# Kernel optimization log

Hardware: AMD Instinct MI355X
Metric: run time of the kernel (lower is better)

The kernel has to match this reference:

```python
import jax, jax.numpy as jnp
import numpy as np

N_NODES = 100000


def _sage_conv(x, edge_index, W_l, b_l, W_r):
    # PyG SAGEConv (aggr='mean', root_weight=True, normalize=False):
    # out = lin_l(mean_{j in N(i)} x_j) + lin_r(x_i)
    src, dst = edge_index[0], edge_index[1]
    n = x.shape[0]
    agg = jax.ops.segment_sum(x[src], dst, num_segments=n)
    cnt = jax.ops.segment_sum(jnp.ones((src.shape[0],), x.dtype), dst, num_segments=n)
    agg = agg / jnp.maximum(cnt, 1.0)[:, None]
    return agg @ W_l + b_l + x @ W_r


def setup_inputs() -> dict:
    key = jax.random.key(0)
    ks = jax.random.split(key, 12)
    in_dim, hidden = 384, 128
    x = jax.random.normal(ks[0], (N_NODES, in_dim), dtype=jnp.float32)
    edge_index = jax.random.randint(ks[1], (2, 3200000), 0, N_NODES, dtype=jnp.int32)
    pos_edge_label_index = jax.random.randint(ks[2], (2, 500000), 0, N_NODES, dtype=jnp.int32)
    neg_edge_label_index = jax.random.randint(ks[3], (2, 500000), 0, N_NODES, dtype=jnp.int32)
    s1 = 1.0 / np.sqrt(in_dim)
    s2 = 1.0 / np.sqrt(hidden)
    return {
        "x": x,
        "edge_index": edge_index,
        "pos_edge_label_index": pos_edge_label_index,
        "neg_edge_label_index": neg_edge_label_index,
        "W_l1": jax.random.uniform(ks[4], (in_dim, hidden), jnp.float32, -s1, s1),
        "b_l1": jnp.zeros((hidden,), jnp.float32),
        "W_r1": jax.random.uniform(ks[5], (in_dim, hidden), jnp.float32, -s1, s1),
        "W_l2": jax.random.uniform(ks[6], (hidden, hidden), jnp.float32, -s2, s2),
        "b_l2": jnp.zeros((hidden,), jnp.float32),
        "W_r2": jax.random.uniform(ks[7], (hidden, hidden), jnp.float32, -s2, s2),
        "W_lin": jax.random.uniform(ks[8], (2 * hidden, 1), jnp.float32, -s2, s2),
        "b_lin": jnp.zeros((1,), jnp.float32),
    }


def reference(x, edge_index, pos_edge_label_index, neg_edge_label_index,
              W_l1, b_l1, W_r1, W_l2, b_l2, W_r2, W_lin, b_lin):
    h = _sage_conv(x, edge_index, W_l1, b_l1, W_r1)
    h = jax.nn.relu(h)
    h = _sage_conv(h, edge_index, W_l2, b_l2, W_r2)

    def score(idx):
        pair = jnp.concatenate([h[idx[0]], h[idx[1]]], axis=1)  # [E, 2*hidden]
        return (pair @ W_lin + b_lin).reshape(-1)

    return score(pos_edge_label_index), score(neg_edge_label_index)
```

## Files before the change

kernel.cpp:

```cpp
#include <hip/hip_runtime.h>

#define IN_DIM 384
#define HID    128
#define NPB    256
#define BCAP   16384
#define LCAP   10240

#define AS1 __attribute__((address_space(1)))
#define AS3 __attribute__((address_space(3)))

typedef _Float16 half8 __attribute__((ext_vector_type(8)));
typedef _Float16 half2t __attribute__((ext_vector_type(2)));
typedef __fp16 fp16x2 __attribute__((ext_vector_type(2)));
typedef float floatx4 __attribute__((ext_vector_type(4)));
typedef float floatx2 __attribute__((ext_vector_type(2)));

__global__ void zero_i32(int* __restrict__ p, int n) {
  int i = blockIdx.x * 256 + threadIdx.x;
  if (i < n) p[i] = 0;
}

__global__ __launch_bounds__(512) void partition_kernel(
    const int* __restrict__ src, const int* __restrict__ dst, int E, int nB,
    int* __restrict__ bCur, unsigned* __restrict__ bucketData) {
  __shared__ int hist[391];
  __shared__ int gbase[391];
  const int t = threadIdx.x;
  const int b0 = blockIdx.x * 8192;

  for (int i = t; i < nB; i += 512) hist[i] = 0;
  __syncthreads();
#pragma unroll
  for (int i = 0; i < 16; ++i) {
    int e = b0 + i * 512 + t;
    if (e < E) atomicAdd(&hist[dst[e] >> 8], 1);
  }
  __syncthreads();
  for (int i = t; i < nB; i += 512) {
    int h = hist[i];
    gbase[i] = h ? (i * BCAP + atomicAdd(&bCur[i], h)) : 0;
    hist[i] = 0;
  }
  __syncthreads();
#pragma unroll
  for (int i = 0; i < 16; ++i) {
    int e = b0 + i * 512 + t;
    if (e < E) {
      int d = dst[e];
      int b = d >> 8;
      int r = atomicAdd(&hist[b], 1);
      bucketData[gbase[b] + r] = ((unsigned)(d & 255) << 17) | (unsigned)src[e];
    }
  }
}

__global__ __launch_bounds__(1024) void node_sort3(
    const unsigned* __restrict__ bucketData, const int* __restrict__ bCur,
    int N, int* __restrict__ sorted_src, int* __restrict__ rs, int* __restrict__ re) {
  extern __shared__ unsigned sdata[];
  __shared__ int hist[NPB];
  __shared__ int s[NPB];
  __shared__ int cur[NPB];
  const int b = blockIdx.x;
  const int t = threadIdx.x;
  const int start = b * BCAP;
  const int fill = bCur[b];
  if (t < NPB) hist[t] = 0;
  __syncthreads();
  for (int i = t; i < fill; i += 1024) {
    unsigned d = bucketData[start + i];
    if (i < LCAP) sdata[i] = d;
    atomicAdd(&hist[d >> 17], 1);
  }
  __syncthreads();
  int v = 0;
  if (t < NPB) { v = hist[t]; s[t] = v; }
  __syncthreads();
  for (int off = 1; off < NPB; off <<= 1) {
    int y = (t < NPB && t >= off) ? s[t - off] : 0;
    __syncthreads();
    if (t < NPB) s[t] += y;
    __syncthreads();
  }
  if (t < NPB) {
    int excl = s[t] - v;
    const int node = b * NPB + t;
    if (node < N) {
      rs[node] = start + excl;
      re[node] = start + excl + v;
    }
    cur[t] = start + excl;
  }
  __syncthreads();
  for (int i = t; i < fill; i += 1024) {
    unsigned d = (i < LCAP) ? sdata[i] : bucketData[start + i];
    int p = atomicAdd(&cur[d >> 17], 1);
    sorted_src[p] = (int)(d & 0x1FFFF);
  }
}

__global__ void pack_w2(const float* __restrict__ Wl, const float* __restrict__ Wr,
                        _Float16* __restrict__ Bp) {
  const float* __restrict__ W = blockIdx.z ? Wr : Wl;
  const int tn = blockIdx.x;
  const int ks = blockIdx.y;
  const int KS = gridDim.y;
  const int lane = threadIdx.x;
  const int n = tn * 16 + (lane & 15);
  const int kb = ks * 32 + (lane >> 4) * 8;
  half8 v;
#pragma unroll
  for (int j = 0; j < 8; ++j) v[j] = (_Float16)W[(size_t)(kb + j) * HID + n];
  *(half8*)(Bp + (((size_t)(blockIdx.z * 8 + tn) * KS + ks) * 64 + lane) * 8) = v;
}

__device__ inline half2t cvt_pk(float a, float b) {
  fp16x2 r = __builtin_amdgcn_cvt_pkrtz(a, b);
  union { fp16x2 f; half2t h; } c;
  c.f = r;
  return c.h;
}

__global__ __launch_bounds__(512) void gemm_f32a(
    const float* __restrict__ A, int M,
    const _Float16* __restrict__ Bp,
    unsigned char* __restrict__ y8, _Float16* __restrict__ z1) {
  __shared__ float As[128 * 32];

  const int K = IN_DIM, KS = IN_DIM / 32;
  const int tid = threadIdx.x;
  const int lane = tid & 63;
  const int wid = tid >> 6;
  const int quad = lane >> 4;
  const int lm = lane & 15;
  const int row0 = (wid & 1) * 64;
  const int ct0 = (wid >> 1) * 4;
  const int blockRow = blockIdx.x * 128;

  const int srow = lane >> 3;
  const int scol = ((lane & 7) ^ (srow & 7)) * 4;
  const int grow0 = min(blockRow + wid * 16 + srow, M - 1);
  const int grow1 = min(blockRow + wid * 16 + 8 + srow, M - 1);

  floatx4 acc[16];
#pragma unroll
  for (int i = 0; i < 16; ++i) {
    acc[i][0] = 0.f; acc[i][1] = 0.f; acc[i][2] = 0.f; acc[i][3] = 0.f;
  }

  for (int ks = 0; ks < KS; ++ks) {
    const int k0 = ks * 32;
    __syncthreads();
    __builtin_amdgcn_global_load_lds(
        (const AS1 void*)(A + (size_t)grow0 * K + k0 + scol),
        (AS3 void*)(As + (wid * 16) * 32), 16, 0, 0);
    __builtin_amdgcn_global_load_lds(
        (const AS1 void*)(A + (size_t)grow1 * K + k0 + scol),
        (AS3 void*)(As + (wid * 16 + 8) * 32), 16, 0, 0);

    half8 bf[4];
#pragma unroll
    for (int ct = 0; ct < 4; ++ct)
      bf[ct] = *(const half8*)(Bp + (((size_t)(ct0 + ct) * KS + ks) * 64 + lane) * 8);

    __syncthreads();

    half8 af[4];
#pragma unroll
    for (int rt = 0; rt < 4; ++rt) {
      const int row = row0 + rt * 16 + lm;
      const int sw = row & 7;
      const floatx4 fA = *(const floatx4*)&As[(row * 8 + ((quad * 2) ^ sw)) * 4];
      const floatx4 fB = *(const floatx4*)&As[(row * 8 + ((quad * 2 + 1) ^ sw)) * 4];
      half2t h01 = cvt_pk(fA[0], fA[1]);
      half2t h23 = cvt_pk(fA[2], fA[3]);
      half2t h45 = cvt_pk(fB[0], fB[1]);
      half2t h67 = cvt_pk(fB[2], fB[3]);
      half8 a;
      a[0] = h01[0]; a[1] = h01[1]; a[2] = h23[0]; a[3] = h23[1];
      a[4] = h45[0]; a[5] = h45[1]; a[6] = h67[0]; a[7] = h67[1];
      af[rt] = a;
    }
#pragma unroll
    for (int rt = 0; rt < 4; ++rt)
#pragma unroll
      for (int ct = 0; ct < 4; ++ct)
        acc[rt * 4 + ct] =
            __builtin_amdgcn_mfma_f32_16x16x32_f16(af[rt], bf[ct], acc[rt * 4 + ct], 0, 0, 0);
  }

#pragma unroll
  for (int rt = 0; rt < 4; ++rt) {
#pragma unroll
    for (int r = 0; r < 4; ++r) {
      const int gm = blockRow + row0 + rt * 16 + quad * 4 + r;
      if (gm < M) {
#pragma unroll
        for (int ct = 0; ct < 4; ++ct) {
          const int tn = ct0 + ct;
          const float v = acc[rt * 4 + ct][r];
          if (tn < 8) {
            int p = __builtin_amdgcn_cvt_pk_fp8_f32(v, v, 0, false);
            y8[(size_t)gm * 128 + tn * 16 + lm] = (unsigned char)(p & 0xFF);
          } else {
            z1[(size_t)gm * 128 + (tn - 8) * 16 + lm] = (_Float16)v;
          }
        }
      }
    }
  }
}

__global__ __launch_bounds__(512) void gemm_f16a(
    const _Float16* __restrict__ A, int M,
    const _Float16* __restrict__ Bp, _Float16* __restrict__ C) {
  __shared__ _Float16 As[128 * 32];

  const int K = HID, KS = HID / 32;
  const int tid = threadIdx.x;
  const int lane = tid & 63;
  const int wid = tid >> 6;
  const int quad = lane >> 4;
  const int lm = lane & 15;
  const int row0 = (wid & 1) * 64;
  const int ct0 = (wid >> 1) * 4;
  const int blockRow = blockIdx.x * 128;

  const int srow = lane >> 2;
  const int scol = ((lane & 3) ^ ((lane >> 3) & 3)) * 8;
  const int grow = min(blockRow + wid * 16 + srow, M - 1);

  floatx4 acc[16];
#pragma unroll
  for (int i = 0; i < 16; ++i) {
    acc[i][0] = 0.f; acc[i][1] = 0.f; acc[i][2] = 0.f; acc[i][3] = 0.f;
  }

  for (int ks = 0; ks < KS; ++ks) {
    const int k0 = ks * 32;
    __syncthreads();
    __builtin_amdgcn_global_load_lds(
        (const AS1 void*)(A + (size_t)grow * K + k0 + scol),
        (AS3 void*)(As + (wid * 16) * 32), 16, 0, 0);

    half8 bf[4];
#pragma unroll
    for (int ct = 0; ct < 4; ++ct)
      bf[ct] = *(const half8*)(Bp + (((size_t)(ct0 + ct) * KS + ks) * 64 + lane) * 8);

    __syncthreads();

    half8 af[4];
#pragma unroll
    for (int rt = 0; rt < 4; ++rt) {
      const int row = row0 + rt * 16 + lm;
      const int cg = quad ^ ((row >> 1) & 3);
      af[rt] = *(const half8*)&As[(row * 4 + cg) * 8];
    }
#pragma unroll
    for (int rt = 0; rt < 4; ++rt)
#pragma unroll
      for (int ct = 0; ct < 4; ++ct)
        acc[rt * 4 + ct] =
            __builtin_amdgcn_mfma_f32_16x16x32_f16(af[rt], bf[ct], acc[rt * 4 + ct], 0, 0, 0);
  }

#pragma unroll
  for (int rt = 0; rt < 4; ++rt) {
#pragma unroll
    for (int r = 0; r < 4; ++r) {
      const int gm = blockRow + row0 + rt * 16 + quad * 4 + r;
      if (gm < M) {
#pragma unroll
        for (int ct = 0; ct < 4; ++ct)
          C[(size_t)gm * 256 + (ct0 + ct) * 16 + lm] = (_Float16)acc[rt * 4 + ct][r];
      }
    }
  }
}

__device__ inline float2 upk(unsigned u) {
  union { unsigned v; _Float16 h[2]; } c; c.v = u;
  return make_float2((float)c.h[0], (float)c.h[1]);
}
__device__ inline half2t as_h2(unsigned u) {
  union { unsigned v; half2t h; } c; c.v = u;
  return c.h;
}
__device__ inline unsigned as_u32(half2t h) {
  union { half2t h; unsigned v; } c; c.h = h;
  return c.v;
}
__device__ inline unsigned pkadd(unsigned a, unsigned b) {
  return as_u32(as_h2(a) + as_h2(b));
}
__device__ inline void pkacc4(uint4& A, const uint4& v) {
  A.x = pkadd(A.x, v.x); A.y = pkadd(A.y, v.y);
  A.z = pkadd(A.z, v.z); A.w = pkadd(A.w, v.w);
}

struct f32acc8 { floatx2 a, b, c, d; };
__device__ inline void f8acc(f32acc8& A, uint2 v) {
  A.a += __builtin_amdgcn_cvt_pk_f32_fp8(v.x, false);
  A.b += __builtin_amdgcn_cvt_pk_f32_fp8(v.x, true);
  A.c += __builtin_amdgcn_cvt_pk_f32_fp8(v.y, false);
  A.d += __builtin_amdgcn_cvt_pk_f32_fp8(v.y, true);
}
__device__ inline void f8merge(f32acc8& A, const f32acc8& B) {
  A.a += B.a; A.b += B.b; A.c += B.c; A.d += B.d;
}

__device__ inline f32acc8 gather_rows8(const unsigned char* __restrict__ y8,
                                       const int* __restrict__ sorted_src,
                                       int start, int end, int cl, int slot) {
  f32acc8 A0; A0.a = 0.f; A0.b = 0.f; A0.c = 0.f; A0.d = 0.f;
  f32acc8 A1 = A0;
  int k = start + slot;
  for (; k + 12 < end; k += 16) {
    int s0 = sorted_src[k];
    int s1 = sorted_src[k + 4];
    int s2 = sorted_src[k + 8];
    int s3 = sorted_src[k + 12];
    uint2 v0 = *(const uint2*)(y8 + (size_t)s0 * 128 + cl * 8);
    uint2 v1 = *(const uint2*)(y8 + (size_t)s1 * 128 + cl * 8);
    uint2 v2 = *(const uint2*)(y8 + (size_t)s2 * 128 + cl * 8);
    uint2 v3 = *(const uint2*)(y8 + (size_t)s3 * 128 + cl * 8);
    f8acc(A0, v0);
    f8acc(A1, v1);
    f8acc(A0, v2);
    f8acc(A1, v3);
  }
  if (k + 4 < end) {
    int s0 = sorted_src[k];
    int s1 = sorted_src[k + 4];
    uint2 v0 = *(const uint2*)(y8 + (size_t)s0 * 128 + cl * 8);
    uint2 v1 = *(const uint2*)(y8 + (size_t)s1 * 128 + cl * 8);
    f8acc(A0, v0);
    f8acc(A1, v1);
    k += 8;
  }
  if (k < end) {
    uint2 v = *(const uint2*)(y8 + (size_t)sorted_src[k] * 128 + cl * 8);
    f8acc(A0, v);
  }
  f8merge(A0, A1);
#pragma unroll
  for (int off = 16; off < 64; off <<= 1) {
    f32acc8 o;
    o.a[0] = __shfl_xor(A0.a[0], off, 64); o.a[1] = __shfl_xor(A0.a[1], off, 64);
    o.b[0] = __shfl_xor(A0.b[0], off, 64); o.b[1] = __shfl_xor(A0.b[1], off, 64);
    o.c[0] = __shfl_xor(A0.c[0], off, 64); o.c[1] = __shfl_xor(A0.c[1], off, 64);
    o.d[0] = __shfl_xor(A0.d[0], off, 64); o.d[1] = __shfl_xor(A0.d[1], off, 64);
    f8merge(A0, o);
  }
  return A0;
}

__global__ __launch_bounds__(256) void agg_relu8(
    const unsigned char* __restrict__ y8, const unsigned* __restrict__ z1u,
    const int* __restrict__ sorted_src,
    const int* __restrict__ rs, const int* __restrict__ re,
    const float* __restrict__ bias, unsigned* __restrict__ h1u, int N) {
  const int w = threadIdx.x >> 6;
  const int lane = threadIdx.x & 63;
  const int cl = lane & 15;
  const int slot = lane >> 4;
  const int node = blockIdx.x * 4 + w;
  if (node >= N) return;
  const int start = rs[node];
  const int end = re[node];
  f32acc8 A = gather_rows8(y8, sorted_src, start, end, cl, slot);
  if (slot == 0) {
    const int deg = end - start;
    const float inv = 1.f / (float)max(deg, 1);
    uint4 z4 = *(const uint4*)(z1u + (size_t)node * 64 + cl * 4);
    const unsigned zv[4] = {z4.x, z4.y, z4.z, z4.w};
    const floatx2 av[4] = {A.a, A.b, A.c, A.d};
    unsigned ov[4];
#pragma unroll
    for (int q = 0; q < 4; ++q) {
      const int c = cl * 8 + q * 2;
      float2 z = upk(zv[q]);
      float vx = fmaxf(av[q][0] * inv + bias[c] + z.x, 0.f);
      float vy = fmaxf(av[q][1] * inv + bias[c + 1] + z.y, 0.f);
      union { unsigned v; _Float16 h[2]; } cc;
      cc.h[0] = (_Float16)vx; cc.h[1] = (_Float16)vy;
      ov[q] = cc.v;
    }
    uint4 o;
    o.x = ov[0]; o.y = ov[1]; o.z = ov[2]; o.w = ov[3];
    *(uint4*)(h1u + (size_t)node * 64 + cl * 4) = o;
  }
}

__device__ inline uint4 gather_rows(const unsigned* __restrict__ yzu,
                                    const int* __restrict__ sorted_src,
                                    int start, int end, int cl, int slot) {
  uint4 A0 = make_uint4(0u, 0u, 0u, 0u);
  uint4 A1 = A0;
  int k = start + slot;
  for (; k + 12 < end; k += 16) {
    int s0 = sorted_src[k];
    int s1 = sorted_src[k + 4];
    int s2 = sorted_src[k + 8];
    int s3 = sorted_src[k + 12];
    uint4 v0 = *(const uint4*)(yzu + (size_t)s0 * 128 + cl * 4);
    uint4 v1 = *(const uint4*)(yzu + (size_t)s1 * 128 + cl * 4);
    uint4 v2 = *(const uint4*)(yzu + (size_t)s2 * 128 + cl * 4);
    uint4 v3 = *(const uint4*)(yzu + (size_t)s3 * 128 + cl * 4);
    pkacc4(A0, v0);
    pkacc4(A1, v1);
    pkacc4(A0, v2);
    pkacc4(A1, v3);
  }
  if (k + 4 < end) {
    int s0 = sorted_src[k];
    int s1 = sorted_src[k + 4];
    uint4 v0 = *(const uint4*)(yzu + (size_t)s0 * 128 + cl * 4);
    uint4 v1 = *(const uint4*)(yzu + (size_t)s1 * 128 + cl * 4);
    pkacc4(A0, v0);
    pkacc4(A1, v1);
    k += 8;
  }
  if (k < end) {
    int s = sorted_src[k];
    uint4 v = *(const uint4*)(yzu + (size_t)s * 128 + cl * 4);
    pkacc4(A0, v);
  }
  pkacc4(A0, A1);
#pragma unroll
  for (int off = 16; off < 64; off <<= 1) {
    uint4 o;
    o.x = (unsigned)__shfl_xor((int)A0.x, off, 64);
    o.y = (unsigned)__shfl_xor((int)A0.y, off, 64);
    o.z = (unsigned)__shfl_xor((int)A0.z, off, 64);
    o.w = (unsigned)__shfl_xor((int)A0.w, off, 64);
    pkacc4(A0, o);
  }
  return A0;
}

__global__ __launch_bounds__(256) void agg_score16(
    const unsigned* __restrict__ yzu, const int* __restrict__ sorted_src,
    const int* __restrict__ rs, const int* __restrict__ re,
    const float* __restrict__ bias, const float* __restrict__ Wlin,
    float* __restrict__ sa, float* __restrict__ sb, int N) {
  const int w = threadIdx.x >> 6;
  const int lane = threadIdx.x & 63;
  const int cl = lane & 15;
  const int slot = lane >> 4;
  const int node = blockIdx.x * 4 + w;
  if (node >= N) return;
  const int start = rs[node];
  const int end = re[node];
  uint4 A = gather_rows(yzu, sorted_src, start, end, cl, slot);
  const int deg = end - start;
  const float inv = 1.f / (float)max(deg, 1);
  uint4 z4 = *(const uint4*)(yzu + (size_t)node * 128 + 64 + cl * 4);
  const unsigned av[4] = {A.x, A.y, A.z, A.w};
  const unsigned zv[4] = {z4.x, z4.y, z4.z, z4.w};
  float pa = 0.f, pb = 0.f;
#pragma unroll
  for (int q = 0; q < 4; ++q) {
    const int cp = cl * 4 + q;
    float2 a = upk(av[q]);
    float2 z = upk(zv[q]);
    float hx = a.x * inv + bias[2 * cp] + z.x;
    float hy = a.y * inv + bias[2 * cp + 1] + z.y;
    pa += hx * Wlin[2 * cp] + hy * Wlin[2 * cp + 1];
    pb += hx * Wlin[128 + 2 * cp] + hy * Wlin[129 + 2 * cp];
  }
#pragma unroll
  for (int off = 1; off < 16; off <<= 1) {
    pa += __shfl_xor(pa, off, 64);
    pb += __shfl_xor(pb, off, 64);
  }
  if (lane == 0) {
    sa[node] = pa;
    sb[node] = pb;
  }
}

__global__ void score2(const int* __restrict__ pos, const int* __restrict__ neg,
                       int Ep, int En,
                       const float* __restrict__ sa, const float* __restrict__ sb,
                       const float* __restrict__ blin, float* __restrict__ out) {
  int e = blockIdx.x * 256 + threadIdx.x;
  if (e < Ep) {
    out[e] = sa[pos[e]] + sb[pos[Ep + e]] + blin[0];
  } else if (e < Ep + En) {
    int i = e - Ep;
    out[Ep + i] = sa[neg[i]] + sb[neg[En + i]] + blin[0];
  }
}

extern "C" void kernel_launch(void* const* d_in, const int* in_sizes, int n_in,
                              void* d_out, int out_size, void* d_ws, size_t ws_size,
                              hipStream_t stream) {
  (void)n_in; (void)out_size; (void)ws_size;
  const float* x    = (const float*)d_in[0];
  const int*   ei   = (const int*)d_in[1];
  const int*   pos  = (const int*)d_in[2];
  const int*   neg  = (const int*)d_in[3];
  const float* Wl1  = (const float*)d_in[4];
  const float* bl1  = (const float*)d_in[5];
  const float* Wr1  = (const float*)d_in[6];
  const float* Wl2  = (const float*)d_in[7];
  const float* bl2  = (const float*)d_in[8];
  const float* Wr2  = (const float*)d_in[9];
  const float* Wlin = (const float*)d_in[10];
  const float* blin = (const float*)d_in[11];

  const int N  = in_sizes[0] / IN_DIM;
  const int E  = in_sizes[1] / 2;
  const int Ep = in_sizes[2] / 2;
  const int En = in_sizes[3] / 2;
  const int* e_src = ei;
  const int* e_dst = ei + E;

  char* ws = (char*)d_ws;
  size_t off = 0;
  auto carve = [&](size_t bytes) -> char* {
    char* p = ws + off;
    off += (bytes + 255) & ~(size_t)255;
    return p;
  };
  const int nB = (N + NPB - 1) / NPB;
  const int KS1 = IN_DIM / 32;
  const int KS2 = HID / 32;

  int*      rs     = (int*)carve((size_t)N * 4);
  int*      re     = (int*)carve((size_t)N * 4);
  int*      bCur   = (int*)carve(512 * 4);
  unsigned* bData  = (unsigned*)carve((size_t)nB * BCAP * 4);
  int*      sorted = (int*)carve((size_t)nB * BCAP * 4);
  float*    sa     = (float*)carve((size_t)N * 4);
  float*    sb     = (float*)carve((size_t)N * 4);
  _Float16* Bp1    = (_Float16*)carve((size_t)16 * KS1 * 64 * 8 * 2);
  _Float16* Bp2    = (_Float16*)carve((size_t)16 * KS2 * 64 * 8 * 2);
  _Float16* yz     = (_Float16*)carve((size_t)N * 256 * 2);
  _Float16* h1     = (_Float16*)carve((size_t)N * 128 * 2);

  unsigned char* y8 = (unsigned char*)yz;
  _Float16*      z1 = (_Float16*)(y8 + (size_t)N * 128);

  const int gemmBlocks = (N + 127) / 128;
  const int partBlocks = (E + 8191) / 8192;

  hipLaunchKernelGGL(zero_i32, dim3(2), dim3(256), 0, stream, bCur, 512);
  hipLaunchKernelGGL(partition_kernel, dim3(partBlocks), dim3(512), 0, stream,
                     e_src, e_dst, E, nB, bCur, bData);
  hipLaunchKernelGGL(node_sort3, dim3(nB), dim3(1024), LCAP * 4, stream,
                     bData, bCur, N, sorted, rs, re);

  hipLaunchKernelGGL(pack_w2, dim3(8, KS1, 2), dim3(64), 0, stream, Wl1, Wr1, Bp1);
  hipLaunchKernelGGL(pack_w2, dim3(8, KS2, 2), dim3(64), 0, stream, Wl2, Wr2, Bp2);

  hipLaunchKernelGGL(gemm_f32a, dim3(gemmBlocks), dim3(512), 0, stream,
                     x, N, Bp1, y8, z1);
  hipLaunchKernelGGL(agg_relu8, dim3((N + 3) / 4), dim3(256), 0, stream,
                     y8, (const unsigned*)z1, sorted, rs, re, bl1, (unsigned*)h1, N);
  hipLaunchKernelGGL(gemm_f16a, dim3(gemmBlocks), dim3(512), 0, stream,
                     h1, N, Bp2, yz);
  hipLaunchKernelGGL(agg_score16, dim3((N + 3) / 4), dim3(256), 0, stream,
                     (const unsigned*)yz, sorted, rs, re, bl2, Wlin, sa, sb, N);

  float* out = (float*)d_out;
  hipLaunchKernelGGL(score2, dim3((Ep + En + 255) / 256), dim3(256), 0, stream,
                     pos, neg, Ep, En, sa, sb, blin, out);
}
```

Baseline: 553.9 us.

## Fold layer-2 weights into the final linear to collapse second conv to scalars

Layer 2 is linear and is followed directly by the scoring linear, so Wl2·Wlin, Wr2·Wlin and bl2·Wlin are precomputed into small vectors. The first aggregation kernel now dots h1 with these vectors to produce two scalars per node. The second aggregation then gathers only a float2 per neighbor instead of 128-wide fp16 rows. This removes the second GEMM, the h1 write, and the wide second gather. The change reorders floating-point sums and shifts the h1 result from fp16 to fp32 precision.

Measured after the change: 476.1 us. 1.16x faster.

```diff
diff --git a/kernel.cpp b/kernel.cpp
--- a/kernel.cpp
+++ b/kernel.cpp
@@ -112,6 +112,29 @@
 #pragma unroll
   for (int j = 0; j < 8; ++j) v[j] = (_Float16)W[(size_t)(kb + j) * HID + n];
   *(half8*)(Bp + (((size_t)(blockIdx.z * 8 + tn) * KS + ks) * 64 + lane) * 8) = v;
+}
+
+__global__ __launch_bounds__(128) void pack_uv(
+    const float* __restrict__ Wl2, const float* __restrict__ Wr2,
+    const float* __restrict__ bl2, const float* __restrict__ Wlin,
+    float* __restrict__ uv) {
+  const int i = threadIdx.x;
+  float ua = 0.f, ub = 0.f, va = 0.f, vb = 0.f;
+  for (int o = 0; o < 128; ++o) {
+    float wa = Wlin[o], wb = Wlin[128 + o];
+    float l = Wl2[i * 128 + o], r = Wr2[i * 128 + o];
+    ua += l * wa; ub += l * wb;
+    va += r * wa; vb += r * wb;
+  }
+  uv[i] = ua; uv[128 + i] = ub; uv[256 + i] = va; uv[384 + i] = vb;
+  if (i == 0) {
+    float ca = 0.f, cb = 0.f;
+    for (int o = 0; o < 128; ++o) {
+      ca += bl2[o] * Wlin[o];
+      cb += bl2[o] * Wlin[128 + o];
+    }
+    uv[512] = ca; uv[513] = cb;
+  }
 }
 
 __device__ inline half2t cvt_pk(float a, float b) {
@@ -211,92 +234,9 @@
   }
 }
 
-__global__ __launch_bounds__(512) void gemm_f16a(
-    const _Float16* __restrict__ A, int M,
-    const _Float16* __restrict__ Bp, _Float16* __restrict__ C) {
-  __shared__ _Float16 As[128 * 32];
-
-  const int K = HID, KS = HID / 32;
-  const int tid = threadIdx.x;
-  const int lane = tid & 63;
-  const int wid = tid >> 6;
-  const int quad = lane >> 4;
-  const int lm = lane & 15;
-  const int row0 = (wid & 1) * 64;
-  const int ct0 = (wid >> 1) * 4;
-  const int blockRow = blockIdx.x * 128;
-
-  const int srow = lane >> 2;
-  const int scol = ((lane & 3) ^ ((lane >> 3) & 3)) * 8;
-  const int grow = min(blockRow + wid * 16 + srow, M - 1);
-
-  floatx4 acc[16];
-#pragma unroll
-  for (int i = 0; i < 16; ++i) {
-    acc[i][0] = 0.f; acc[i][1] = 0.f; acc[i][2] = 0.f; acc[i][3] = 0.f;
-  }
-
-  for (int ks = 0; ks < KS; ++ks) {
-    const int k0 = ks * 32;
-    __syncthreads();
-    __builtin_amdgcn_global_load_lds(
-        (const AS1 void*)(A + (size_t)grow * K + k0 + scol),
-        (AS3 void*)(As + (wid * 16) * 32), 16, 0, 0);
-
-    half8 bf[4];
-#pragma unroll
-    for (int ct = 0; ct < 4; ++ct)
-      bf[ct] = *(const half8*)(Bp + (((size_t)(ct0 + ct) * KS + ks) * 64 + lane) * 8);
-
-    __syncthreads();
-
-    half8 af[4];
-#pragma unroll
-    for (int rt = 0; rt < 4; ++rt) {
-      const int row = row0 + rt * 16 + lm;
-      const int cg = quad ^ ((row >> 1) & 3);
-      af[rt] = *(const half8*)&As[(row * 4 + cg) * 8];
-    }
-#pragma unroll
-    for (int rt = 0; rt < 4; ++rt)
-#pragma unroll
-      for (int ct = 0; ct < 4; ++ct)
-        acc[rt * 4 + ct] =
-            __builtin_amdgcn_mfma_f32_16x16x32_f16(af[rt], bf[ct], acc[rt * 4 + ct], 0, 0, 0);
-  }
-
-#pragma unroll
-  for (int rt = 0; rt < 4; ++rt) {
-#pragma unroll
-    for (int r = 0; r < 4; ++r) {
-      const int gm = blockRow + row0 + rt * 16 + quad * 4 + r;
-      if (gm < M) {
-#pragma unroll
-        for (int ct = 0; ct < 4; ++ct)
-          C[(size_t)gm * 256 + (ct0 + ct) * 16 + lm] = (_Float16)acc[rt * 4 + ct][r];
-      }
-    }
-  }
-}
-
 __device__ inline float2 upk(unsigned u) {
   union { unsigned v; _Float16 h[2]; } c; c.v = u;
   return make_float2((float)c.h[0], (float)c.h[1]);
-}
-__device__ inline half2t as_h2(unsigned u) {
-  union { unsigned v; half2t h; } c; c.v = u;
-  return c.h;
-}
-__device__ inline unsigned as_u32(half2t h) {
-  union { half2t h; unsigned v; } c; c.h = h;
-  return c.v;
-}
-__device__ inline unsigned pkadd(unsigned a, unsigned b) {
-  return as_u32(as_h2(a) + as_h2(b));
-}
-__device__ inline void pkacc4(uint4& A, const uint4& v) {
-  A.x = pkadd(A.x, v.x); A.y = pkadd(A.y, v.y);
-  A.z = pkadd(A.z, v.z); A.w = pkadd(A.w, v.w);
 }
 
 struct f32acc8 { floatx2 a, b, c, d; };
@@ -356,11 +296,12 @@
   return A0;
 }
 
-__global__ __launch_bounds__(256) void agg_relu8(
+__global__ __launch_bounds__(256) void agg_relu8_dot(
     const unsigned char* __restrict__ y8, const unsigned* __restrict__ z1u,
     const int* __restrict__ sorted_src,
     const int* __restrict__ rs, const int* __restrict__ re,
-    const float* __restrict__ bias, unsigned* __restrict__ h1u, int N) {
+    const float* __restrict__ bias, const float* __restrict__ uv,
+    float2* __restrict__ t, float2* __restrict__ r, int N) {
   const int w = threadIdx.x >> 6;
   const int lane = threadIdx.x & 63;
   const int cl = lane & 15;
@@ -376,108 +317,67 @@
     uint4 z4 = *(const uint4*)(z1u + (size_t)node * 64 + cl * 4);
     const unsigned zv[4] = {z4.x, z4.y, z4.z, z4.w};
     const floatx2 av[4] = {A.a, A.b, A.c, A.d};
-    unsigned ov[4];
+    float hv[8];
 #pragma unroll
     for (int q = 0; q < 4; ++q) {
       const int c = cl * 8 + q * 2;
       float2 z = upk(zv[q]);
-      float vx = fmaxf(av[q][0] * inv + bias[c] + z.x, 0.f);
-      float vy = fmaxf(av[q][1] * inv + bias[c + 1] + z.y, 0.f);
-      union { unsigned v; _Float16 h[2]; } cc;
-      cc.h[0] = (_Float16)vx; cc.h[1] = (_Float16)vy;
-      ov[q] = cc.v;
-    }
-    uint4 o;
-    o.x = ov[0]; o.y = ov[1]; o.z = ov[2]; o.w = ov[3];
-    *(uint4*)(h1u + (size_t)node * 64 + cl * 4) = o;
-  }
-}
-
-__device__ inline uint4 gather_rows(const unsigned* __restrict__ yzu,
-                                    const int* __restrict__ sorted_src,
-                                    int start, int end, int cl, int slot) {
-  uint4 A0 = make_uint4(0u, 0u, 0u, 0u);
-  uint4 A1 = A0;
-  int k = start + slot;
-  for (; k + 12 < end; k += 16) {
-    int s0 = sorted_src[k];
-    int s1 = sorted_src[k + 4];
-    int s2 = sorted_src[k + 8];
-    int s3 = sorted_src[k + 12];
-    uint4 v0 = *(const uint4*)(yzu + (size_t)s0 * 128 + cl * 4);
-    uint4 v1 = *(const uint4*)(yzu + (size_t)s1 * 128 + cl * 4);
-    uint4 v2 = *(const uint4*)(yzu + (size_t)s2 * 128 + cl * 4);
-    uint4 v3 = *(const uint4*)(yzu + (size_t)s3 * 128 + cl * 4);
-    pkacc4(A0, v0);
-    pkacc4(A1, v1);
-    pkacc4(A0, v2);
-    pkacc4(A1, v3);
-  }
-  if (k + 4 < end) {
-    int s0 = sorted_src[k];
-    int s1 = sorted_src[k + 4];
-    uint4 v0 = *(const uint4*)(yzu + (size_t)s0 * 128 + cl * 4);
-    uint4 v1 = *(const uint4*)(yzu + (size_t)s1 * 128 + cl * 4);
-    pkacc4(A0, v0);
-    pkacc4(A1, v1);
-    k += 8;
-  }
-  if (k < end) {
-    int s = sorted_src[k];
-    uint4 v = *(const uint4*)(yzu + (size_t)s * 128 + cl * 4);
-    pkacc4(A0, v);
-  }
-  pkacc4(A0, A1);
-#pragma unroll
-  for (int off = 16; off < 64; off <<= 1) {
-    uint4 o;
-    o.x = (unsigned)__shfl_xor((int)A0.x, off, 64);
-    o.y = (unsigned)__shfl_xor((int)A0.y, off, 64);
-    o.z = (unsigned)__shfl_xor((int)A0.z, off, 64);
-    o.w = (unsigned)__shfl_xor((int)A0.w, off, 64);
-    pkacc4(A0, o);
-  }
-  return A0;
-}
-
-__global__ __launch_bounds__(256) void agg_score16(
-    const unsigned* __restrict__ yzu, const int* __restrict__ sorted_src,
+      hv[2 * q]     = fmaxf(av[q][0] * inv + bias[c] + z.x, 0.f);
+      hv[2 * q + 1] = fmaxf(av[q][1] * inv + bias[c + 1] + z.y, 0.f);
+    }
+    float ta = 0.f, tb = 0.f, ra = 0.f, rb = 0.f;
+#pragma unroll
+    for (int j = 0; j < 8; ++j) {
+      const int c = cl * 8 + j;
+      ta += hv[j] * uv[c];
+      tb += hv[j] * uv[128 + c];
+      ra += hv[j] * uv[256 + c];
+      rb += hv[j] * uv[384 + c];
+    }
+#pragma unroll
+    for (int off = 1; off < 16; off <<= 1) {
+      ta += __shfl_xor(ta, off, 64);
+      tb += __shfl_xor(tb, off, 64);
+      ra += __shfl_xor(ra, off, 64);
+      rb += __shfl_xor(rb, off, 64);
+    }
+    if (cl == 0) {
+      t[node] = make_float2(ta, tb);
+      r[node] = make_float2(ra + uv[512], rb + uv[513]);
+    }
+  }
+}
+
+__global__ __launch_bounds__(256) void agg_t(
+    const float2* __restrict__ t, const int* __restrict__ sorted_src,
     const int* __restrict__ rs, const int* __restrict__ re,
-    const float* __restrict__ bias, const float* __restrict__ Wlin,
+    const float2* __restrict__ r,
     float* __restrict__ sa, float* __restrict__ sb, int N) {
   const int w = threadIdx.x >> 6;
   const int lane = threadIdx.x & 63;
-  const int cl = lane & 15;
-  const int slot = lane >> 4;
-  const int node = blockIdx.x * 4 + w;
+  const int es = lane & 15;
+  const int ns = lane >> 4;
+  const int node = blockIdx.x * 16 + w * 4 + ns;
   if (node >= N) return;
   const int start = rs[node];
   const int end = re[node];
-  uint4 A = gather_rows(yzu, sorted_src, start, end, cl, slot);
-  const int deg = end - start;
-  const float inv = 1.f / (float)max(deg, 1);
-  uint4 z4 = *(const uint4*)(yzu + (size_t)node * 128 + 64 + cl * 4);
-  const unsigned av[4] = {A.x, A.y, A.z, A.w};
-  const unsigned zv[4] = {z4.x, z4.y, z4.z, z4.w};
-  float pa = 0.f, pb = 0.f;
-#pragma unroll
-  for (int q = 0; q < 4; ++q) {
-    const int cp = cl * 4 + q;
-    float2 a = upk(av[q]);
-    float2 z = upk(zv[q]);
-    float hx = a.x * inv + bias[2 * cp] + z.x;
-    float hy = a.y * inv + bias[2 * cp + 1] + z.y;
-    pa += hx * Wlin[2 * cp] + hy * Wlin[2 * cp + 1];
-    pb += hx * Wlin[128 + 2 * cp] + hy * Wlin[129 + 2 * cp];
+  float a = 0.f, b = 0.f;
+  for (int k = start + es; k < end; k += 16) {
+    float2 v = t[sorted_src[k]];
+    a += v.x;
+    b += v.y;
   }
 #pragma unroll
   for (int off = 1; off < 16; off <<= 1) {
-    pa += __shfl_xor(pa, off, 64);
-    pb += __shfl_xor(pb, off, 64);
-  }
-  if (lane == 0) {
-    sa[node] = pa;
-    sb[node] = pb;
+    a += __shfl_xor(a, off, 64);
+    b += __shfl_xor(b, off, 64);
+  }
+  if (es == 0) {
+    const int deg = end - start;
+    const float inv = 1.f / (float)max(deg, 1);
+    float2 rr = r[node];
+    sa[node] = a * inv + rr.x;
+    sb[node] = b * inv + rr.y;
   }
 }
 
@@ -527,22 +427,20 @@
   };
   const int nB = (N + NPB - 1) / NPB;
   const int KS1 = IN_DIM / 32;
-  const int KS2 = HID / 32;
-
-  int*      rs     = (int*)carve((size_t)N * 4);
-  int*      re     = (int*)carve((size_t)N * 4);
-  int*      bCur   = (int*)carve(512 * 4);
-  unsigned* bData  = (unsigned*)carve((size_t)nB * BCAP * 4);
-  int*      sorted = (int*)carve((size_t)nB * BCAP * 4);
-  float*    sa     = (float*)carve((size_t)N * 4);
-  float*    sb     = (float*)carve((size_t)N * 4);
-  _Float16* Bp1    = (_Float16*)carve((size_t)16 * KS1 * 64 * 8 * 2);
-  _Float16* Bp2    = (_Float16*)carve((size_t)16 * KS2 * 64 * 8 * 2);
-  _Float16* yz     = (_Float16*)carve((size_t)N * 256 * 2);
-  _Float16* h1     = (_Float16*)carve((size_t)N * 128 * 2);
-
-  unsigned char* y8 = (unsigned char*)yz;
-  _Float16*      z1 = (_Float16*)(y8 + (size_t)N * 128);
+
+  int*           rs     = (int*)carve((size_t)N * 4);
+  int*           re     = (int*)carve((size_t)N * 4);
+  int*           bCur   = (int*)carve(512 * 4);
+  unsigned*      bData  = (unsigned*)carve((size_t)nB * BCAP * 4);
+  int*           sorted = (int*)carve((size_t)nB * BCAP * 4);
+  float*         sa     = (float*)carve((size_t)N * 4);
+  float*         sb     = (float*)carve((size_t)N * 4);
+  _Float16*      Bp1    = (_Float16*)carve((size_t)16 * KS1 * 64 * 8 * 2);
+  float*         uv     = (float*)carve(516 * 4);
+  float2*        tbuf   = (float2*)carve((size_t)N * 8);
+  float2*        rbuf   = (float2*)carve((size_t)N * 8);
+  unsigned char* y8     = (unsigned char*)carve((size_t)N * 128);
+  _Float16*      z1     = (_Float16*)carve((size_t)N * 128 * 2);
 
   const int gemmBlocks = (N + 127) / 128;
   const int partBlocks = (E + 8191) / 8192;
@@ -554,16 +452,14 @@
                      bData, bCur, N, sorted, rs, re);
 
   hipLaunchKernelGGL(pack_w2, dim3(8, KS1, 2), dim3(64), 0, stream, Wl1, Wr1, Bp1);
-  hipLaunchKernelGGL(pack_w2, dim3(8, KS2, 2), dim3(64), 0, stream, Wl2, Wr2, Bp2);
+  hipLaunchKernelGGL(pack_uv, dim3(1), dim3(128), 0, stream, Wl2, Wr2, bl2, Wlin, uv);
 
   hipLaunchKernelGGL(gemm_f32a, dim3(gemmBlocks), dim3(512), 0, stream,
                      x, N, Bp1, y8, z1);
-  hipLaunchKernelGGL(agg_relu8, dim3((N + 3) / 4), dim3(256), 0, stream,
-                     y8, (const unsigned*)z1, sorted, rs, re, bl1, (unsigned*)h1, N);
-  hipLaunchKernelGGL(gemm_f16a, dim3(gemmBlocks), dim3(512), 0, stream,
-                     h1, N, Bp2, yz);
-  hipLaunchKernelGGL(agg_score16, dim3((N + 3) / 4), dim3(256), 0, stream,
-                     (const unsigned*)yz, sorted, rs, re, bl2, Wlin, sa, sb, N);
+  hipLaunchKernelGGL(agg_relu8_dot, dim3((N + 3) / 4), dim3(256), 0, stream,
+                     y8, (const unsigned*)z1, sorted, rs, re, bl1, uv, tbuf, rbuf, N);
+  hipLaunchKernelGGL(agg_t, dim3((N + 15) / 16), dim3(256), 0, stream,
+                     tbuf, sorted, rs, re, rbuf, sa, sb, N);
 
   float* out = (float*)d_out;
   hipLaunchKernelGGL(score2, dim3((Ep + En + 255) / 256), dim3(256), 0, stream,
```
